# Optimization experiments

Hardware: AMD Instinct MI355X
Metric: run time of the kernel (lower is better)

The kernel has to match this reference:

```python
import jax, jax.numpy as jnp
import numpy as np

HIDDEN = 450
DEPTH = 8
VOCAB = 780
N_NODES = 5120
N_MESS = 10241


def setup_inputs() -> dict:
    key = jax.random.key(0)
    ks = jax.random.split(key, 16)
    s = 0.05  # weight scale for numerical sanity
    return {
        "fnode": jax.random.randint(ks[0], (N_NODES,), 0, VOCAB),
        "fmess": jax.random.randint(ks[1], (N_MESS,), 0, N_NODES),
        "node_graph": jax.random.randint(ks[2], (N_NODES, 6), 0, N_MESS),
        "mess_graph": jax.random.randint(ks[3], (N_MESS, 5), 0, N_MESS),
        "emb": jax.random.normal(ks[4], (VOCAB, HIDDEN), jnp.float32),
        "Wz": jax.random.normal(ks[5], (2 * HIDDEN, HIDDEN), jnp.float32) * s,
        "bz": jnp.zeros((HIDDEN,), jnp.float32),
        "Wr": jax.random.normal(ks[6], (HIDDEN, HIDDEN), jnp.float32) * s,
        "Ur": jax.random.normal(ks[7], (HIDDEN, HIDDEN), jnp.float32) * s,
        "bu": jnp.zeros((HIDDEN,), jnp.float32),
        "Wh": jax.random.normal(ks[8], (2 * HIDDEN, HIDDEN), jnp.float32) * s,
        "bh": jnp.zeros((HIDDEN,), jnp.float32),
        "Wo": jax.random.normal(ks[9], (2 * HIDDEN, HIDDEN), jnp.float32) * s,
        "bo": jnp.zeros((HIDDEN,), jnp.float32),
        "batch_size": 128,
    }


def _gru(fmess_e, mess_graph, Wz, bz, Wr, Ur, bu, Wh, bh):
    # JTNN graph-GRU: depth-unrolled message updates over the message graph.
    M = fmess_e.shape[0]
    h0 = jnp.zeros((M, HIDDEN), fmess_e.dtype)
    mask = jnp.ones((M, 1), fmess_e.dtype).at[0].set(0.0)  # slot 0 = dummy message
    r1 = (fmess_e @ Wr)[:, None, :]  # loop-invariant W_r(fmess), [M,1,H]

    def step(h, _):
        h_nei = h[mess_graph]                     # [M,K,H] gather (index_select_ND)
        sum_h = h_nei.sum(axis=1)                 # [M,H]
        z = jax.nn.sigmoid(jnp.concatenate([fmess_e, sum_h], -1) @ Wz + bz)
        r = jax.nn.sigmoid(r1 + h_nei @ Ur + bu)  # [M,K,H]
        sum_gh = (r * h_nei).sum(axis=1)
        pre_h = jnp.tanh(jnp.concatenate([fmess_e, sum_gh], -1) @ Wh + bh)
        h = ((1.0 - z) * sum_h + z * pre_h) * mask
        return h, None

    h, _ = jax.lax.scan(step, h0, None, length=DEPTH)
    return h


def reference(fnode, fmess, node_graph, mess_graph, emb, Wz, bz, Wr, Ur, bu,
              Wh, bh, Wo, bo, batch_size):
    x = emb[fnode]                    # [N,H] embedding gather
    fmess_e = x[fmess]                # [M,H] message input features
    h = _gru(fmess_e, mess_graph, Wz, bz, Wr, Ur, bu, Wh, bh)  # [M,H]
    mess_nei = h[node_graph]          # [N,Kn,H]
    node_vecs = jnp.concatenate([x, mess_nei.sum(axis=1)], -1)  # [N,2H]
    node_vecs = jax.nn.relu(node_vecs @ Wo + bo)                # outputNN
    # uniform scope: every tree has N_NODES // batch_size nodes -> static reshape
    tree_vecs = node_vecs.reshape(batch_size, -1, HIDDEN)       # [B,L,H]
    messages = jnp.zeros((mess_graph.shape[0], HIDDEN), node_vecs.dtype)
    return (tree_vecs, messages)
```

## Files before the change

### kernel.cpp

```cpp
#include <hip/hip_runtime.h>
#include <cstdint>
#include <cstddef>

#define H 450
#define H2 900
#define KP 480
#define KP2 960
#define NMESS 10241
#define NNODE 5120
#define MPAD 10368
#define SPP1 960
#define SPP2 1920
#define PPSZ ((size_t)MPAD * SPP1)
#define KM 5
#define KN 6
#define LDCH 960

typedef __attribute__((ext_vector_type(8))) short short8;
typedef __attribute__((ext_vector_type(4))) float f32x4;

__device__ __forceinline__ short bf16rne(float f) {
  union { float f; unsigned u; } x; x.f = f;
  unsigned u = x.u;
  u += 0x7FFF + ((u >> 16) & 1);
  return (short)(u >> 16);
}
__device__ __forceinline__ float bf16tof(short s) {
  union { float f; unsigned u; } x;
  x.u = ((unsigned)(unsigned short)s) << 16;
  return x.f;
}
__device__ __forceinline__ void bf16split(float v, short& hi, short& lo) {
  hi = bf16rne(v);
  lo = bf16rne(v - bf16tof(hi));
}
__device__ __forceinline__ float sigmoidf_(float x) {
  return 1.f / (1.f + __expf(-x));
}

__device__ __forceinline__ size_t ppix(int row, int k, int spp) {
  return (size_t)row * spp + ((k >> 5) << 6) + (k & 31);
}

__device__ __forceinline__ void gll16(const short* g, short* l) {
  __builtin_amdgcn_global_load_lds(
      (const __attribute__((address_space(1))) void*)g,
      (__attribute__((address_space(3))) void*)l, 16, 0, 0);
}

#define BM 64
#define BN 64
#define BK 32

struct SmemT { short As[2][64][64]; short Bs[2][64][64]; };

__device__ __forceinline__ void xcd_swz(int gx, int gy, int& bm, int& bn) {
  const int nwg = gx * gy;
  int lid = blockIdx.y * gx + blockIdx.x;
  const int q = nwg >> 3, r = nwg & 7;
  const int xcd = lid & 7, seq = lid >> 3;
  int sid = (xcd < r) ? (xcd * (q + 1) + seq)
                      : (r * (q + 1) + (xcd - r) * q + seq);
  bm = (sid / gx) * BM;
  bn = (sid % gx) * BN;
}

template<int ACT, int OUT>
__device__ __forceinline__ void gemm_core(
    SmemT& sm, const short* __restrict__ Apk, int Kpad,
    const short* __restrict__ Bpk,
    const float* __restrict__ bias,
    float* C, int ldc, short* Cs,
    const short* __restrict__ E1, const short* __restrict__ E2,
    const short* __restrict__ E3,
    int M, int N, int bm, int bn)
{
  const int tid  = threadIdx.x;
  const int lane = tid & 63;
  const int wid  = tid >> 6;
  const int wm   = (wid >> 1) * 32;
  const int wn   = (wid & 1) * 32;
  const int l15  = lane & 15;
  const int s8   = (lane >> 4) * 8;
  const int rr0  = (lane >> 4) * 4;
  const int spp  = Kpad * 2;

  const int lr = lane >> 3;
  const int sl = lane & 7;
  const int t0 = sl ^ lr;
  const short* src[4];
#pragma unroll
  for (int qq = 0; qq < 4; ++qq) {
    const int rrow = wid * 32 + qq * 8 + lr;
    const bool isA = rrow < 64;
    const int grow = isA ? (bm + rrow) : (bn + rrow - 64);
    src[qq] = (isA ? Apk : Bpk) + (size_t)grow * spp + t0 * 8;
  }
  const int nk = Kpad / BK;

  f32x4 acc[2][2];
#pragma unroll
  for (int i = 0; i < 2; ++i)
#pragma unroll
    for (int j = 0; j < 2; ++j)
#pragma unroll
      for (int t = 0; t < 4; ++t) acc[i][j][t] = 0.f;

  auto STAGE = [&](int b, int koff) {
#pragma unroll
    for (int qq = 0; qq < 4; ++qq) {
      const int r0 = wid * 32 + qq * 8;
      short* d = (r0 < 64) ? &sm.As[b][r0][0] : &sm.Bs[b][r0 - 64][0];
      gll16(src[qq] + koff, d);
    }
  };

  STAGE(0, 0);
  __syncthreads();
  int cur = 0;
  for (int t = 0; t < nk; ++t) {
    if (t + 1 < nk) STAGE(cur ^ 1, (t + 1) * 64);
    short8 ah[2], al[2], bh[2], bl[2];
#pragma unroll
    for (int i = 0; i < 2; ++i) {
      const int rA = wm + i*16 + l15;
      const int xr = (rA & 7) << 3;
      ah[i] = *(const short8*)&sm.As[cur][rA][(s8)      ^ xr];
      al[i] = *(const short8*)&sm.As[cur][rA][(s8 + 32) ^ xr];
    }
#pragma unroll
    for (int j = 0; j < 2; ++j) {
      const int rB = wn + j*16 + l15;
      const int xr = (rB & 7) << 3;
      bh[j] = *(const short8*)&sm.Bs[cur][rB][(s8)      ^ xr];
      bl[j] = *(const short8*)&sm.Bs[cur][rB][(s8 + 32) ^ xr];
    }
    __builtin_amdgcn_s_setprio(1);
#pragma unroll
    for (int j = 0; j < 2; ++j)
#pragma unroll
      for (int i = 0; i < 2; ++i) {
        acc[i][j] = __builtin_amdgcn_mfma_f32_16x16x32_bf16(ah[i], bh[j], acc[i][j], 0, 0, 0);
        acc[i][j] = __builtin_amdgcn_mfma_f32_16x16x32_bf16(al[i], bh[j], acc[i][j], 0, 0, 0);
        acc[i][j] = __builtin_amdgcn_mfma_f32_16x16x32_bf16(ah[i], bl[j], acc[i][j], 0, 0, 0);
      }
    __builtin_amdgcn_s_setprio(0);
    __syncthreads();
    cur ^= 1;
  }

#pragma unroll
  for (int j = 0; j < 2; ++j) {
    int col = bn + wn + j*16 + l15;
    if (col >= N) continue;
    float bv = ((OUT == 0 || OUT == 3) && bias) ? bias[col] : 0.f;
#pragma unroll
    for (int i = 0; i < 2; ++i) {
      int row0 = bm + wm + i*16 + rr0;
#pragma unroll
      for (int rr = 0; rr < 4; ++rr) {
        int row = row0 + rr;
        if (row >= M) continue;
        float v = acc[i][j][rr] + bv;
        if (OUT == 0) {
          if (ACT == 1) v = fmaxf(v, 0.f);
          C[(size_t)row * ldc + col] = v;
        } else if (OUT == 3) {
          Cs[(size_t)row * ldc + col] = bf16rne(v);
        } else {
          float tz = bf16tof(E2[(size_t)row * 480 + col]);
          float cz = bf16tof(E1[(size_t)row * LDCH + col]);
          float ch = bf16tof(E1[(size_t)row * LDCH + 450 + col]);
          size_t op = ppix(row, col, SPP1);
          float sm2 = bf16tof(E3[op]) + bf16tof(E3[op + 32]);
          float z   = sigmoidf_(cz + tz);
          float pre = tanhf(ch + v);
          float hv  = (1.f - z) * sm2 + z * pre;
          if (row == 0) hv = 0.f;
          short hi, lo; bf16split(hv, hi, lo);
          Cs[op] = hi; Cs[op + 32] = lo;
        }
      }
    }
  }
}

template<int ACT>
__global__ __launch_bounds__(256, 5)
void gemm4(const short* __restrict__ Apk, int Kpad,
           const short* __restrict__ Bpk,
           const float* __restrict__ bias,
           float* C, int ldc, int M, int N)
{
  __shared__ SmemT sm;
  int bm, bn; xcd_swz(gridDim.x, gridDim.y, bm, bn);
  gemm_core<ACT, 0>(sm, Apk, Kpad, Bpk, bias, C, ldc, nullptr,
                    nullptr, nullptr, nullptr, M, N, bm, bn);
}

__global__ __launch_bounds__(256, 5)
void gemm4_b(const short* __restrict__ Apk, int Kpad,
             const short* __restrict__ Bpk,
             const float* __restrict__ bias,
             short* Cs, int ldcs, int M, int N)
{
  __shared__ SmemT sm;
  int bm, bn; xcd_swz(gridDim.x, gridDim.y, bm, bn);
  gemm_core<0, 3>(sm, Apk, Kpad, Bpk, bias, nullptr, ldcs, Cs,
                  nullptr, nullptr, nullptr, M, N, bm, bn);
}

__global__ __launch_bounds__(256, 5)
void gemm4_thc(const short* __restrict__ Apk,
               const short* __restrict__ Bpk,
               const short* __restrict__ CHb,
               const short* __restrict__ tzb,
               const short* __restrict__ shP,
               short* hP)
{
  __shared__ SmemT sm;
  int bm, bn; xcd_swz(gridDim.x, gridDim.y, bm, bn);
  gemm_core<0, 4>(sm, Apk, KP, Bpk, nullptr, nullptr, 0, hP,
                  CHb, tzb, shP, NMESS, H, bm, bn);
}

__global__ __launch_bounds__(256)
void k_wT(const float* __restrict__ W, int Kreal,
          short* __restrict__ Bt, int Kpad, int rmax) {
  __shared__ float T[32][33];
  const int tx = threadIdx.x & 31;
  const int ty = threadIdx.x >> 5;
  const int k0 = blockIdx.x * 32;
  const int c0 = blockIdx.y * 32;
  const int spp = Kpad * 2;
#pragma unroll
  for (int i = 0; i < 4; ++i) {
    int k = k0 + ty + i*8, c = c0 + tx;
    T[ty + i*8][tx] = (k < Kreal && c < H) ? W[(size_t)k * H + c] : 0.f;
  }
  __syncthreads();
#pragma unroll
  for (int i = 0; i < 4; ++i) {
    int c = c0 + ty + i*8, k = k0 + tx;
    if (k < Kpad && c < rmax) {
      short hi, lo;
      bf16split(T[tx][ty + i*8], hi, lo);
      size_t o = ppix(c, k, spp);
      Bt[o] = hi; Bt[o + 32] = lo;
    }
  }
}

__global__ void k_biascat(const float* __restrict__ bz, const float* __restrict__ bh,
                          float* __restrict__ biasI) {
  int c = blockIdx.x * blockDim.x + threadIdx.x;
  if (c >= 900) return;
  biasI[c] = (c < 450) ? bz[c] : bh[c - 450];
}


__global__ void k_build_idx(const int* __restrict__ fnode,
                            const int* __restrict__ fmess,
                            int* __restrict__ idxM) {
  int m = blockIdx.x * blockDim.x + threadIdx.x;
  if (m < NMESS) idxM[m] = fnode[fmess[m]];
}

__global__ void k_embsplit(const float* __restrict__ emb,
                           const int* __restrict__ idxM,
                           short* __restrict__ eP) {
  int m = blockIdx.x, j = threadIdx.x * 2;
  if (j >= KP) return;
  size_t o = ppix(m, j, SPP1);
  if (j < H) {
    float2 v = *(const float2*)&emb[(size_t)idxM[m] * H + j];
    short2 h2, l2;
    bf16split(v.x, h2.x, l2.x); bf16split(v.y, h2.y, l2.y);
    *(short2*)&eP[o] = h2; *(short2*)&eP[o + 32] = l2;
  } else {
    short2 z2; z2.x = 0; z2.y = 0;
    *(short2*)&eP[o] = z2; *(short2*)&eP[o + 32] = z2;
  }
}

__global__ void k_h1(const short* __restrict__ CHb, short* __restrict__ hP) {
  int m = blockIdx.x, j = threadIdx.x * 2;
  if (j >= KP) return;
  size_t oP = ppix(m, j, SPP1);
  if (j < H) {
    size_t oc = (size_t)m * LDCH + j;
    short2 cz2 = *(const short2*)&CHb[oc];
    short2 ch2 = *(const short2*)&CHb[oc + 450];
    float v0 = sigmoidf_(bf16tof(cz2.x)) * tanhf(bf16tof(ch2.x));
    float v1 = sigmoidf_(bf16tof(cz2.y)) * tanhf(bf16tof(ch2.y));
    if (m == 0) { v0 = 0.f; v1 = 0.f; }
    short2 h2, l2;
    bf16split(v0, h2.x, l2.x); bf16split(v1, h2.y, l2.y);
    *(short2*)&hP[oP] = h2; *(short2*)&hP[oP + 32] = l2;
  } else {
    short2 z2; z2.x = 0; z2.y = 0;
    *(short2*)&hP[oP] = z2; *(short2*)&hP[oP + 32] = z2;
  }
}

__global__ void k_gather3(const short* __restrict__ hP,
                          const short* __restrict__ GU,
                          const short* __restrict__ r1b,
                          const int* __restrict__ mg,
                          short* __restrict__ shP, short* __restrict__ ghP,
                          short* __restrict__ tzb) {
  int m = blockIdx.x, j = threadIdx.x * 2;
  if (j >= KP) return;
  size_t o = ppix(m, j, SPP1);
  if (j >= H) {
    short2 z2; z2.x = 0; z2.y = 0;
    *(short2*)&shP[o] = z2; *(short2*)&shP[o + 32] = z2;
    *(short2*)&ghP[o] = z2; *(short2*)&ghP[o + 32] = z2;
    return;
  }
  const int* e = mg + (size_t)m * KM;
  short2 rb2 = *(const short2*)&r1b[(size_t)m * 480 + j];
  float rb0 = bf16tof(rb2.x), rb1 = bf16tof(rb2.y);
  float s0 = 0.f, s1 = 0.f, t0 = 0.f, t1 = 0.f, u0 = 0.f, u1 = 0.f;
#pragma unroll
  for (int k = 0; k < KM; ++k) {
    int ek = e[k];
    size_t oP = ppix(ek, j, SPP1);
    size_t oG = (size_t)ek * LDCH + j;
    short2 gv = *(const short2*)&GU[oG];
    short2 uv = *(const short2*)&GU[oG + 450];
    short2 ph = *(const short2*)&hP[oP];
    short2 pl = *(const short2*)&hP[oP + 32];
    float h0 = bf16tof(ph.x) + bf16tof(pl.x);
    float h1 = bf16tof(ph.y) + bf16tof(pl.y);
    s0 += h0;                                  s1 += h1;
    t0 += sigmoidf_(rb0 + bf16tof(gv.x)) * h0; t1 += sigmoidf_(rb1 + bf16tof(gv.y)) * h1;
    u0 += bf16tof(uv.x);                       u1 += bf16tof(uv.y);
  }
  short2 h2, l2;
  bf16split(s0, h2.x, l2.x); bf16split(s1, h2.y, l2.y);
  *(short2*)&shP[o] = h2; *(short2*)&shP[o + 32] = l2;
  bf16split(t0, h2.x, l2.x); bf16split(t1, h2.y, l2.y);
  *(short2*)&ghP[o] = h2; *(short2*)&ghP[o + 32] = l2;
  short2 tz2; tz2.x = bf16rne(u0); tz2.y = bf16rne(u1);
  *(short2*)&tzb[(size_t)m * 480 + j] = tz2;
}

__global__ void k_nodecat(const float* __restrict__ emb,
                          const int* __restrict__ fnode,
                          const short* __restrict__ hP,
                          const int* __restrict__ ng,
                          short* __restrict__ Apk) {
  int n = blockIdx.x, t = threadIdx.x, j = t * 2;
  if (j < H) {
    float2 v = *(const float2*)&emb[(size_t)fnode[n] * H + j];
    short2 h2, l2;
    bf16split(v.x, h2.x, l2.x); bf16split(v.y, h2.y, l2.y);
    size_t o = ppix(n, j, SPP2);
    *(short2*)&Apk[o] = h2; *(short2*)&Apk[o + 32] = l2;

    const int* e = ng + (size_t)n * KN;
    float s0 = 0.f, s1 = 0.f;
#pragma unroll
    for (int k = 0; k < KN; ++k) {
      size_t oP = ppix(e[k], j, SPP1);
      short2 ph = *(const short2*)&hP[oP];
      short2 pl = *(const short2*)&hP[oP + 32];
      s0 += bf16tof(ph.x) + bf16tof(pl.x);
      s1 += bf16tof(ph.y) + bf16tof(pl.y);
    }
    bf16split(s0, h2.x, l2.x); bf16split(s1, h2.y, l2.y);
    o = ppix(n, 450 + j, SPP2);
    *(short2*)&Apk[o] = h2; *(short2*)&Apk[o + 32] = l2;
  }
  if (t < 30) {
    int c = 900 + t * 2;
    short2 z2; z2.x = 0; z2.y = 0;
    size_t o = ppix(n, c, SPP2);
    *(short2*)&Apk[o] = z2; *(short2*)&Apk[o + 32] = z2;
  }
}


extern "C" void kernel_launch(void* const* d_in, const int* in_sizes, int n_in,
                              void* d_out, int out_size, void* d_ws, size_t ws_size,
                              hipStream_t stream) {
  (void)in_sizes; (void)n_in; (void)out_size; (void)ws_size;

  const int*   fnode      = (const int*)d_in[0];
  const int*   fmess      = (const int*)d_in[1];
  const int*   node_graph = (const int*)d_in[2];
  const int*   mess_graph = (const int*)d_in[3];
  const float* emb        = (const float*)d_in[4];
  const float* Wz         = (const float*)d_in[5];
  const float* bz         = (const float*)d_in[6];
  const float* Wr         = (const float*)d_in[7];
  const float* Ur         = (const float*)d_in[8];
  const float* bu         = (const float*)d_in[9];
  const float* Wh         = (const float*)d_in[10];
  const float* bh         = (const float*)d_in[11];
  const float* Wo         = (const float*)d_in[12];
  const float* bo         = (const float*)d_in[13];

  short* P   = (short*)d_ws;
  short* hP  = P;
  short* shP = P + 1 * PPSZ;
  short* ghP = P + 2 * PPSZ;
  short* CHb = P + 3 * PPSZ;
  short* GU  = CHb + (size_t)NMESS * LDCH;
  short* r1b = GU  + (size_t)NMESS * LDCH;
  short* tzb = r1b + (size_t)NMESS * 480;

  char*  scr  = (char*)d_out + (size_t)NNODE * H * 4;
  short* BtI  = (short*)scr;
  short* BtR  = BtI  + (size_t)1408 * SPP1;
  short* BtGU = BtR  + (size_t)512 * SPP1;
  short* BtHH = BtGU + (size_t)1024 * SPP1;
  short* BtO  = BtHH + (size_t)512 * SPP1;
  float* biasI = (float*)(BtO + (size_t)512 * SPP2);
  int*   idxM  = (int*)(biasI + 912);

  k_build_idx<<<(NMESS + 255) / 256, 256, 0, stream>>>(fnode, fmess, idxM);

  dim3 gT(KP / 32, 16), gT2(KP2 / 32, 16);
  k_wT<<<gT,  256, 0, stream>>>(Wz,                  H, BtI,               KP,  512);
  k_wT<<<gT,  256, 0, stream>>>(Wh,                  H, BtI + 450 * SPP1,  KP,  512);
  k_wT<<<gT,  256, 0, stream>>>(Wr,                  H, BtR,               KP,  512);
  k_wT<<<gT,  256, 0, stream>>>(Ur,                  H, BtGU,              KP,  512);
  k_wT<<<gT,  256, 0, stream>>>(Wz + (size_t)H * H,  H, BtGU + 450 * SPP1, KP,  512);
  k_wT<<<gT,  256, 0, stream>>>(Wh + (size_t)H * H,  H, BtHH,              KP,  512);
  k_wT<<<gT2, 256, 0, stream>>>(Wo,                 H2, BtO,               KP2, 512);
  k_biascat<<<4, 256, 0, stream>>>(bz, bh, biasI);

  k_embsplit<<<NMESS, 256, 0, stream>>>(emb, idxM, ghP);

  dim3 gI1(15, MPAD / BM);
  gemm4_b<<<gI1, 256, 0, stream>>>(ghP, KP, BtI, biasI, CHb, LDCH, NMESS, H2);
  dim3 gI2(8, MPAD / BM);
  gemm4_b<<<gI2, 256, 0, stream>>>(ghP, KP, BtR, bu, r1b, 480, NMESS, H);

  k_h1<<<NMESS, 256, 0, stream>>>(CHb, hP);

  dim3 gGU(15, MPAD / BM);
  dim3 gB(8, MPAD / BM);
  for (int d = 1; d < 8; ++d) {
    gemm4_b<<<gGU, 256, 0, stream>>>(hP, KP, BtGU, nullptr, GU, LDCH, NMESS, H2);
    k_gather3<<<NMESS, 256, 0, stream>>>(hP, GU, r1b, mess_graph, shP, ghP, tzb);
    gemm4_thc<<<gB, 256, 0, stream>>>(ghP, BtHH, CHb, tzb, shP, hP);
  }

  k_nodecat<<<NNODE, 256, 0, stream>>>(emb, fnode, hP, node_graph, shP);
  dim3 gF(8, NNODE / BM);
  gemm4<1><<<gF, 256, 0, stream>>>(shP, KP2, BtO, bo, (float*)d_out, H, NNODE, H);

  hipMemsetAsync((float*)d_out + (size_t)NNODE * H, 0, (size_t)NMESS * H * sizeof(float), stream);
}
```

Measured before the change: 937.4 us.

## Replace LDS-staged GEMM tiles with direct global-to-register fragment loads

Removes the shared-memory double buffer, the global_load_lds staging and the per-iteration barriers from the split-bf16 GEMM core. Each wave now loads its MFMA fragments straight from global memory into registers, with two register fragment sets ping-ponged for software pipelining. Launch bounds drop from 5 to 4 waves per SIMD to leave room for the extra registers. Waves in a block no longer share tile loads, so global/L2 traffic per block goes up, and occupancy may fall.

Measured after the change: 2.196 ms. 134% more time.

```diff
diff --git a/kernel.cpp b/kernel.cpp
--- a/kernel.cpp
+++ b/kernel.cpp
@@ -42,17 +42,8 @@
   return (size_t)row * spp + ((k >> 5) << 6) + (k & 31);
 }
 
-__device__ __forceinline__ void gll16(const short* g, short* l) {
-  __builtin_amdgcn_global_load_lds(
-      (const __attribute__((address_space(1))) void*)g,
-      (__attribute__((address_space(3))) void*)l, 16, 0, 0);
-}
-
 #define BM 64
 #define BN 64
-#define BK 32
-
-struct SmemT { short As[2][64][64]; short Bs[2][64][64]; };
 
 __device__ __forceinline__ void xcd_swz(int gx, int gy, int& bm, int& bn) {
   const int nwg = gx * gy;
@@ -65,9 +56,11 @@
   bn = (sid % gx) * BN;
 }
 
+struct Frag { short8 ah[2], al[2], bh[2], bl[2]; };
+
 template<int ACT, int OUT>
 __device__ __forceinline__ void gemm_core(
-    SmemT& sm, const short* __restrict__ Apk, int Kpad,
+    const short* __restrict__ Apk, int Kpad,
     const short* __restrict__ Bpk,
     const float* __restrict__ bias,
     float* C, int ldc, short* Cs,
@@ -85,18 +78,11 @@
   const int rr0  = (lane >> 4) * 4;
   const int spp  = Kpad * 2;
 
-  const int lr = lane >> 3;
-  const int sl = lane & 7;
-  const int t0 = sl ^ lr;
-  const short* src[4];
-#pragma unroll
-  for (int qq = 0; qq < 4; ++qq) {
-    const int rrow = wid * 32 + qq * 8 + lr;
-    const bool isA = rrow < 64;
-    const int grow = isA ? (bm + rrow) : (bn + rrow - 64);
-    src[qq] = (isA ? Apk : Bpk) + (size_t)grow * spp + t0 * 8;
-  }
-  const int nk = Kpad / BK;
+  const short* pa0 = Apk + (size_t)(bm + wm +  0 + l15) * spp + s8;
+  const short* pa1 = Apk + (size_t)(bm + wm + 16 + l15) * spp + s8;
+  const short* pb0 = Bpk + (size_t)(bn + wn +  0 + l15) * spp + s8;
+  const short* pb1 = Bpk + (size_t)(bn + wn + 16 + l15) * spp + s8;
+  const int nk = Kpad / 32;
 
   f32x4 acc[2][2];
 #pragma unroll
@@ -106,48 +92,36 @@
 #pragma unroll
       for (int t = 0; t < 4; ++t) acc[i][j][t] = 0.f;
 
-  auto STAGE = [&](int b, int koff) {
-#pragma unroll
-    for (int qq = 0; qq < 4; ++qq) {
-      const int r0 = wid * 32 + qq * 8;
-      short* d = (r0 < 64) ? &sm.As[b][r0][0] : &sm.Bs[b][r0 - 64][0];
-      gll16(src[qq] + koff, d);
-    }
+  Frag f0, f1;
+  auto LOADF = [&](Frag& f, int t) {
+    const int o = t * 64;
+    f.ah[0] = *(const short8*)(pa0 + o); f.al[0] = *(const short8*)(pa0 + o + 32);
+    f.ah[1] = *(const short8*)(pa1 + o); f.al[1] = *(const short8*)(pa1 + o + 32);
+    f.bh[0] = *(const short8*)(pb0 + o); f.bl[0] = *(const short8*)(pb0 + o + 32);
+    f.bh[1] = *(const short8*)(pb1 + o); f.bl[1] = *(const short8*)(pb1 + o + 32);
   };
-
-  STAGE(0, 0);
-  __syncthreads();
-  int cur = 0;
-  for (int t = 0; t < nk; ++t) {
-    if (t + 1 < nk) STAGE(cur ^ 1, (t + 1) * 64);
-    short8 ah[2], al[2], bh[2], bl[2];
-#pragma unroll
-    for (int i = 0; i < 2; ++i) {
-      const int rA = wm + i*16 + l15;
-      const int xr = (rA & 7) << 3;
-      ah[i] = *(const short8*)&sm.As[cur][rA][(s8)      ^ xr];
-      al[i] = *(const short8*)&sm.As[cur][rA][(s8 + 32) ^ xr];
-    }
-#pragma unroll
-    for (int j = 0; j < 2; ++j) {
-      const int rB = wn + j*16 + l15;
-      const int xr = (rB & 7) << 3;
-      bh[j] = *(const short8*)&sm.Bs[cur][rB][(s8)      ^ xr];
-      bl[j] = *(const short8*)&sm.Bs[cur][rB][(s8 + 32) ^ xr];
-    }
+  auto MF = [&](Frag& f) {
     __builtin_amdgcn_s_setprio(1);
 #pragma unroll
     for (int j = 0; j < 2; ++j)
 #pragma unroll
       for (int i = 0; i < 2; ++i) {
-        acc[i][j] = __builtin_amdgcn_mfma_f32_16x16x32_bf16(ah[i], bh[j], acc[i][j], 0, 0, 0);
-        acc[i][j] = __builtin_amdgcn_mfma_f32_16x16x32_bf16(al[i], bh[j], acc[i][j], 0, 0, 0);
-        acc[i][j] = __builtin_amdgcn_mfma_f32_16x16x32_bf16(ah[i], bl[j], acc[i][j], 0, 0, 0);
+        acc[i][j] = __builtin_amdgcn_mfma_f32_16x16x32_bf16(f.ah[i], f.bh[j], acc[i][j], 0, 0, 0);
+        acc[i][j] = __builtin_amdgcn_mfma_f32_16x16x32_bf16(f.al[i], f.bh[j], acc[i][j], 0, 0, 0);
+        acc[i][j] = __builtin_amdgcn_mfma_f32_16x16x32_bf16(f.ah[i], f.bl[j], acc[i][j], 0, 0, 0);
       }
     __builtin_amdgcn_s_setprio(0);
-    __syncthreads();
-    cur ^= 1;
-  }
+  };
+
+  LOADF(f0, 0);
+  int t = 0;
+  for (; t + 1 < nk; t += 2) {
+    LOADF(f1, t + 1);
+    MF(f0);
+    if (t + 2 < nk) LOADF(f0, t + 2);
+    MF(f1);
+  }
+  if (t < nk) MF(f0);
 
 #pragma unroll
   for (int j = 0; j < 2; ++j) {
@@ -186,31 +160,29 @@
 }
 
 template<int ACT>
-__global__ __launch_bounds__(256, 5)
+__global__ __launch_bounds__(256, 4)
 void gemm4(const short* __restrict__ Apk, int Kpad,
            const short* __restrict__ Bpk,
            const float* __restrict__ bias,
            float* C, int ldc, int M, int N)
 {
-  __shared__ SmemT sm;
   int bm, bn; xcd_swz(gridDim.x, gridDim.y, bm, bn);
-  gemm_core<ACT, 0>(sm, Apk, Kpad, Bpk, bias, C, ldc, nullptr,
+  gemm_core<ACT, 0>(Apk, Kpad, Bpk, bias, C, ldc, nullptr,
                     nullptr, nullptr, nullptr, M, N, bm, bn);
 }
 
-__global__ __launch_bounds__(256, 5)
+__global__ __launch_bounds__(256, 4)
 void gemm4_b(const short* __restrict__ Apk, int Kpad,
              const short* __restrict__ Bpk,
              const float* __restrict__ bias,
              short* Cs, int ldcs, int M, int N)
 {
-  __shared__ SmemT sm;
   int bm, bn; xcd_swz(gridDim.x, gridDim.y, bm, bn);
-  gemm_core<0, 3>(sm, Apk, Kpad, Bpk, bias, nullptr, ldcs, Cs,
+  gemm_core<0, 3>(Apk, Kpad, Bpk, bias, nullptr, ldcs, Cs,
                   nullptr, nullptr, nullptr, M, N, bm, bn);
 }
 
-__global__ __launch_bounds__(256, 5)
+__global__ __launch_bounds__(256, 4)
 void gemm4_thc(const short* __restrict__ Apk,
                const short* __restrict__ Bpk,
                const short* __restrict__ CHb,
@@ -218,9 +190,8 @@
                const short* __restrict__ shP,
                short* hP)
 {
-  __shared__ SmemT sm;
   int bm, bn; xcd_swz(gridDim.x, gridDim.y, bm, bn);
-  gemm_core<0, 4>(sm, Apk, KP, Bpk, nullptr, nullptr, 0, hP,
+  gemm_core<0, 4>(Apk, KP, Bpk, nullptr, nullptr, 0, hP,
                   CHb, tzb, shP, NMESS, H, bm, bn);
 }
 
```
